# Kernel optimization log

Measured on AMD Instinct MI355X. Metric: run time of the kernel, lower is better.

The kernel has to match this reference:

```python
import jax, jax.numpy as jnp
import numpy as np

B, T, D = 2, 4096, 512
H = 8  # heads; head_dim = D // H = 64


def setup_inputs() -> dict:
    key = jax.random.key(0)
    ks = jax.random.split(key, 8)
    s = 0.02
    return {
        "queries": jax.random.normal(ks[0], (B, T, D), jnp.float32),
        "keys": jax.random.normal(ks[1], (B, T, D), jnp.float32),
        "values": jax.random.normal(ks[2], (B, T, D), jnp.float32),
        "Wq": jax.random.normal(ks[3], (D, D), jnp.float32) * s,
        "Wk": jax.random.normal(ks[4], (D, D), jnp.float32) * s,
        "Wv": jax.random.normal(ks[5], (D, D), jnp.float32) * s,
        "Wo": jax.random.normal(ks[6], (D, D), jnp.float32) * s,
        "bo": jnp.zeros((D,), jnp.float32),
    }


def reference(queries, keys, values, Wq, Wk, Wv, Wo, bo):
    # pad_dim = 0 for in_dim=512, n_heads=8, so no padding needed.
    Bq, Tq, _ = queries.shape
    Ts = keys.shape[1]
    hd = D // H
    # torch Linear: x @ W.T
    q = (queries @ Wq.T).reshape(Bq, Tq, H, hd).transpose(0, 2, 1, 3)  # [B,H,T,hd]
    k = (keys @ Wk.T).reshape(Bq, Ts, H, hd).transpose(0, 2, 1, 3)
    v = (values @ Wv.T).reshape(Bq, Ts, H, hd).transpose(0, 2, 1, 3)
    attn = jnp.einsum("bhtd,bhsd->bhts", q, k) / np.sqrt(hd).astype(np.float32)
    attn = jax.nn.softmax(attn, axis=-1)  # [B,H,T,Ts]
    z = jnp.einsum("bhts,bhsd->bhtd", attn, v)
    z = z.transpose(0, 2, 1, 3).reshape(Bq, Tq, D)
    out = z @ Wo.T + bo
    return (out, attn)
```

## Files before the change

kernel.cpp:

```cpp
#include <hip/hip_runtime.h>

typedef __attribute__((ext_vector_type(8))) short bf16x8;
typedef __attribute__((ext_vector_type(8))) unsigned short u16x8;
typedef __attribute__((ext_vector_type(4))) float f32x4;
typedef __attribute__((ext_vector_type(2))) unsigned uint2v;
typedef __attribute__((ext_vector_type(4))) unsigned uint4v;

#define DEVINL __device__ __forceinline__

constexpr int TB = 2;
constexpr int TT = 4096;
constexpr int TD = 512;
constexpr int TH = 8;
constexpr int THD = 64;
constexpr int TM = TB * TT;

DEVINL unsigned short f2b(float f) {
  unsigned u = __builtin_bit_cast(unsigned, f);
  u += 0x7FFFu + ((u >> 16) & 1u);
  return (unsigned short)(u >> 16);
}

DEVINL unsigned cvtpk(float lo, float hi) {
  unsigned r;
  asm("v_cvt_pk_bf16_f32 %0, %1, %2" : "=v"(r) : "v"(lo), "v"(hi));
  return r;
}

DEVINL void lgkm_barrier() {
  asm volatile("s_waitcnt lgkmcnt(0)" ::: "memory");
  __builtin_amdgcn_s_barrier();
  __builtin_amdgcn_sched_barrier(0);
}

__global__ __launch_bounds__(256, 2)
void proj_qkv(const float* __restrict__ Xq, const float* __restrict__ Xk,
              const float* __restrict__ Xv, const float* __restrict__ Wq,
              const float* __restrict__ Wk, const float* __restrict__ Wv,
              unsigned short* __restrict__ qb, unsigned short* __restrict__ kb,
              unsigned short* __restrict__ vt)
{
  constexpr int K = TD, N = TD;
  __shared__ unsigned short As[128][72];
  __shared__ unsigned short Bs[128][72];

  const int z = blockIdx.z;
  const float* X = (z == 0) ? Xq : (z == 1) ? Xk : Xv;
  const float* W = (z == 0) ? Wq : (z == 1) ? Wk : Wv;
  unsigned short* Yb = (z == 0) ? qb : (z == 1) ? kb : vt;
  const bool TR = (z == 2);

  const int t    = threadIdx.x;
  const int lane = t & 63, w = t >> 6;
  const int fr = lane & 15, fq = lane >> 4;
  const int wr = (w >> 1) * 64, wc = (w & 1) * 64;
  const int bm = blockIdx.x * 128, bn = blockIdx.y * 128;
  const int srow = t >> 1;
  const int skh  = (t & 1) * 32;

  f32x4 acc[4][4];
  #pragma unroll
  for (int i = 0; i < 4; ++i)
    #pragma unroll
    for (int j = 0; j < 4; ++j)
      acc[i][j] = f32x4{0.f, 0.f, 0.f, 0.f};

  for (int k0 = 0; k0 < K; k0 += 64) {
    const float* srcA = X + (size_t)(bm + srow) * K + k0 + skh;
    const float* srcB = W + (size_t)(bn + srow) * K + k0 + skh;
    #pragma unroll
    for (int i = 0; i < 4; ++i) {
      float4 a0 = ((const float4*)srcA)[2 * i];
      float4 a1 = ((const float4*)srcA)[2 * i + 1];
      u16x8 oa = {f2b(a0.x), f2b(a0.y), f2b(a0.z), f2b(a0.w),
                  f2b(a1.x), f2b(a1.y), f2b(a1.z), f2b(a1.w)};
      *(u16x8*)&As[srow][skh + i * 8] = oa;
      float4 b0 = ((const float4*)srcB)[2 * i];
      float4 b1 = ((const float4*)srcB)[2 * i + 1];
      u16x8 ob = {f2b(b0.x), f2b(b0.y), f2b(b0.z), f2b(b0.w),
                  f2b(b1.x), f2b(b1.y), f2b(b1.z), f2b(b1.w)};
      *(u16x8*)&Bs[srow][skh + i * 8] = ob;
    }
    __syncthreads();
    #pragma unroll
    for (int kk = 0; kk < 2; ++kk) {
      bf16x8 af[4], bfv[4];
      #pragma unroll
      for (int i = 0; i < 4; ++i)
        af[i] = *(const bf16x8*)&As[wr + i * 16 + fr][kk * 32 + fq * 8];
      #pragma unroll
      for (int j = 0; j < 4; ++j)
        bfv[j] = *(const bf16x8*)&Bs[wc + j * 16 + fr][kk * 32 + fq * 8];
      if (TR) {
        #pragma unroll
        for (int i = 0; i < 4; ++i)
          #pragma unroll
          for (int j = 0; j < 4; ++j)
            acc[i][j] = __builtin_amdgcn_mfma_f32_16x16x32_bf16(bfv[i], af[j], acc[i][j], 0, 0, 0);
      } else {
        #pragma unroll
        for (int i = 0; i < 4; ++i)
          #pragma unroll
          for (int j = 0; j < 4; ++j)
            acc[i][j] = __builtin_amdgcn_mfma_f32_16x16x32_bf16(af[i], bfv[j], acc[i][j], 0, 0, 0);
      }
    }
    __syncthreads();
  }

  if (TR) {
    #pragma unroll
    for (int i = 0; i < 4; ++i)
      #pragma unroll
      for (int j = 0; j < 4; ++j)
        #pragma unroll
        for (int ii = 0; ii < 4; ++ii) {
          const int Nidx = bn + wc + i * 16 + fq * 4 + ii;
          const int Midx = bm + wr + j * 16 + fr;
          const int h = Nidx >> 6, dd = Nidx & (THD - 1);
          const int b = Midx >> 12, tt = Midx & (TT - 1);
          Yb[((size_t)(b * TH + h) * THD + dd) * TT + tt] = f2b(acc[i][j][ii]);
        }
  } else {
    #pragma unroll
    for (int i = 0; i < 4; ++i)
      #pragma unroll
      for (int j = 0; j < 4; ++j)
        #pragma unroll
        for (int ii = 0; ii < 4; ++ii) {
          const int gm = bm + wr + i * 16 + fq * 4 + ii;
          const int gn = bn + wc + j * 16 + fr;
          Yb[(size_t)gm * N + gn] = f2b(acc[i][j][ii]);
        }
  }
}

__global__ __launch_bounds__(256, 2)
void gemm_final(const float* __restrict__ X, const float* __restrict__ W,
                float* __restrict__ Yf, const float* __restrict__ bias)
{
  constexpr int K = TD, N = TD;
  __shared__ unsigned short As[128][72];
  __shared__ unsigned short Bs[128][72];

  const int t    = threadIdx.x;
  const int lane = t & 63, w = t >> 6;
  const int fr = lane & 15, fq = lane >> 4;
  const int wr = (w >> 1) * 64, wc = (w & 1) * 64;
  const int bm = blockIdx.x * 128, bn = blockIdx.y * 128;
  const int srow = t >> 1;
  const int skh  = (t & 1) * 32;

  f32x4 acc[4][4];
  #pragma unroll
  for (int i = 0; i < 4; ++i)
    #pragma unroll
    for (int j = 0; j < 4; ++j)
      acc[i][j] = f32x4{0.f, 0.f, 0.f, 0.f};

  for (int k0 = 0; k0 < K; k0 += 64) {
    const float* srcA = X + (size_t)(bm + srow) * K + k0 + skh;
    const float* srcB = W + (size_t)(bn + srow) * K + k0 + skh;
    #pragma unroll
    for (int i = 0; i < 4; ++i) {
      float4 a0 = ((const float4*)srcA)[2 * i];
      float4 a1 = ((const float4*)srcA)[2 * i + 1];
      u16x8 oa = {f2b(a0.x), f2b(a0.y), f2b(a0.z), f2b(a0.w),
                  f2b(a1.x), f2b(a1.y), f2b(a1.z), f2b(a1.w)};
      *(u16x8*)&As[srow][skh + i * 8] = oa;
      float4 b0 = ((const float4*)srcB)[2 * i];
      float4 b1 = ((const float4*)srcB)[2 * i + 1];
      u16x8 ob = {f2b(b0.x), f2b(b0.y), f2b(b0.z), f2b(b0.w),
                  f2b(b1.x), f2b(b1.y), f2b(b1.z), f2b(b1.w)};
      *(u16x8*)&Bs[srow][skh + i * 8] = ob;
    }
    __syncthreads();
    #pragma unroll
    for (int kk = 0; kk < 2; ++kk) {
      bf16x8 af[4], bfv[4];
      #pragma unroll
      for (int i = 0; i < 4; ++i)
        af[i] = *(const bf16x8*)&As[wr + i * 16 + fr][kk * 32 + fq * 8];
      #pragma unroll
      for (int j = 0; j < 4; ++j)
        bfv[j] = *(const bf16x8*)&Bs[wc + j * 16 + fr][kk * 32 + fq * 8];
      #pragma unroll
      for (int i = 0; i < 4; ++i)
        #pragma unroll
        for (int j = 0; j < 4; ++j)
          acc[i][j] = __builtin_amdgcn_mfma_f32_16x16x32_bf16(af[i], bfv[j], acc[i][j], 0, 0, 0);
    }
    __syncthreads();
  }

  #pragma unroll
  for (int i = 0; i < 4; ++i)
    #pragma unroll
    for (int j = 0; j < 4; ++j)
      #pragma unroll
      for (int ii = 0; ii < 4; ++ii) {
        const int gm = bm + wr + i * 16 + fq * 4 + ii;
        const int gn = bn + wc + j * 16 + fr;
        Yf[(size_t)gm * N + gn] = acc[i][j][ii] + bias[gn];
      }
}

__global__ __launch_bounds__(256, 4)
void attn_pass1(const unsigned short* __restrict__ Qb,
                const unsigned short* __restrict__ Kb,
                const unsigned short* __restrict__ VTg,
                float* __restrict__ Z, float* __restrict__ l2iW)
{
  __shared__ unsigned short Ks[2][32][72];
  __shared__ unsigned short VTs[2][64][40];

  const int t    = threadIdx.x;
  const int lane = t & 63, w = t >> 6;
  const int fr = lane & 15, fq = lane >> 4;

  const int d  = blockIdx.x;
  const int bh = 2 * (d & 7) + ((d >> 3) & 1);
  const int q0 = (d >> 4) * 64;
  const int b  = bh >> 3, h = bh & 7;

  const size_t rowKV  = ((size_t)(b * TT)) * TD + h * THD;
  const size_t vtBase = (size_t)bh * THD * TT;

  const int trK = t >> 3, tcK = (t & 7) * 8;
  const int trV = t >> 2, tcV = (t & 3) * 8;

  auto loadK = [&](int kv0, u16x8& r) {
    r = *(const u16x8*)(Kb + rowKV + (size_t)(kv0 + trK) * TD + tcK);
  };
  auto loadVT = [&](int kv0, u16x8& r) {
    r = *(const u16x8*)(VTg + vtBase + (size_t)trV * TT + kv0 + tcV);
  };
  auto writeK  = [&](int buf, const u16x8& r) { *(u16x8*)&Ks[buf][trK][tcK]  = r; };
  auto writeVT = [&](int buf, const u16x8& r) { *(u16x8*)&VTs[buf][trV][tcV] = r; };

  const unsigned short* qsrc = Qb + ((size_t)(b * TT + q0 + w * 16 + fr)) * TD + h * THD;
  bf16x8 aq[2];
  aq[0] = *(const bf16x8*)(qsrc + fq * 8);
  aq[1] = *(const bf16x8*)(qsrc + 32 + fq * 8);

  constexpr int KVB = 32;
  constexpr int NT = TT / KVB;
  constexpr float K2 = 0.18033688011112042f;

  u16x8 kA, vA, kB, vB;
  {
    u16x8 k0, v0;
    loadK(0, k0); loadVT(0, v0);
    writeK(0, k0); writeVT(0, v0);
    loadK(KVB, kB); loadVT(KVB, vB);
    lgkm_barrier();
  }

  float lsum = 0.f;
  f32x4 accz[4];
  #pragma unroll
  for (int n = 0; n < 4; ++n) accz[n] = f32x4{0.f, 0.f, 0.f, 0.f};

  for (int jp = 0; jp < NT / 2; ++jp) {
    #pragma unroll
    for (int half = 0; half < 2; ++half) {
      const int j = jp * 2 + half;
      const int cur = j & 1;
      if (j + 2 < NT) {
        if (half == 0) { loadK((j + 2) * KVB, kA); loadVT((j + 2) * KVB, vA); }
        else           { loadK((j + 2) * KVB, kB); loadVT((j + 2) * KVB, vB); }
      }
      f32x4 sv[2];
      __builtin_amdgcn_s_setprio(1);
      #pragma unroll
      for (int n = 0; n < 2; ++n) {
        f32x4 s = f32x4{0.f, 0.f, 0.f, 0.f};
        #pragma unroll
        for (int kk = 0; kk < 2; ++kk) {
          bf16x8 ak = *(const bf16x8*)&Ks[cur][n * 16 + fr][kk * 32 + fq * 8];
          s = __builtin_amdgcn_mfma_f32_16x16x32_bf16(ak, aq[kk], s, 0, 0, 0);
        }
        sv[n] = s;
      }
      __builtin_amdgcn_s_setprio(0);
      float p[2][4];
      #pragma unroll
      for (int n = 0; n < 2; ++n)
        #pragma unroll
        for (int i = 0; i < 4; ++i) {
          p[n][i] = __builtin_amdgcn_exp2f(sv[n][i] * K2);
          lsum += p[n][i];
        }
      uint4v pav = {cvtpk(p[0][0], p[0][1]), cvtpk(p[0][2], p[0][3]),
                    cvtpk(p[1][0], p[1][1]), cvtpk(p[1][2], p[1][3])};
      bf16x8 ap = __builtin_bit_cast(bf16x8, pav);
      __builtin_amdgcn_s_setprio(1);
      #pragma unroll
      for (int df = 0; df < 4; ++df) {
        uint2v lo = *(const uint2v*)&VTs[cur][df * 16 + fr][fq * 4];
        uint2v hi = *(const uint2v*)&VTs[cur][df * 16 + fr][16 + fq * 4];
        uint4v bvv = {lo[0], lo[1], hi[0], hi[1]};
        accz[df] = __builtin_amdgcn_mfma_f32_16x16x32_bf16(
            ap, __builtin_bit_cast(bf16x8, bvv), accz[df], 0, 0, 0);
      }
      __builtin_amdgcn_s_setprio(0);
      if (j + 1 < NT) {
        if (half == 0) { writeK(cur ^ 1, kB); writeVT(cur ^ 1, vB); }
        else           { writeK(cur ^ 1, kA); writeVT(cur ^ 1, vA); }
      }
      lgkm_barrier();
    }
  }

  lsum += __shfl_xor(lsum, 16, 64);
  lsum += __shfl_xor(lsum, 32, 64);

  if (fq == 0)
    l2iW[(size_t)bh * TT + q0 + w * 16 + fr] = -__log2f(lsum);

  float rls[4];
  #pragma unroll
  for (int i = 0; i < 4; ++i)
    rls[i] = 1.0f / __shfl(lsum, fq * 4 + i, 64);
  const size_t zbase = ((size_t)(b * TT + q0 + w * 16 + fq * 4)) * TD + h * THD + fr;
  #pragma unroll
  for (int df = 0; df < 4; ++df)
    #pragma unroll
    for (int i = 0; i < 4; ++i)
      Z[zbase + (size_t)i * TD + df * 16] = accz[df][i] * rls[i];
}

__global__ __launch_bounds__(256, 4)
void attn_pass2(const unsigned short* __restrict__ Qb,
                const unsigned short* __restrict__ Kb,
                const float* __restrict__ l2iW,
                float* __restrict__ attnO)
{
  __shared__ unsigned short KsW[4][2][32][72];

  const int t    = threadIdx.x;
  const int lane = t & 63, w = t >> 6;
  const int fr = lane & 15, fq = lane >> 4;

  const int d  = blockIdx.x;
  const int bh = 2 * (d & 7) + ((d >> 3) & 1);
  const int q0 = (d >> 4) * 64;
  const int b  = bh >> 3, h = bh & 7;

  const size_t rowKV = ((size_t)(b * TT)) * TD + h * THD;

  const unsigned short* qsrc = Qb + ((size_t)(b * TT + q0 + w * 16 + fr)) * TD + h * THD;
  bf16x8 aq[2];
  aq[0] = *(const bf16x8*)(qsrc + fq * 8);
  aq[1] = *(const bf16x8*)(qsrc + 32 + fq * 8);

  const float l2i = l2iW[(size_t)bh * TT + q0 + w * 16 + fr];

  constexpr int KVB = 32;
  constexpr int NT = TT / KVB;
  constexpr float K2 = 0.18033688011112042f;

  const int phase = (37 * d + 32 * w) & (NT - 1);
  const int prow = lane >> 3, pcol = (lane & 7) * 8;

  u16x8 sA[4], sB[4];
  auto loadKW = [&](int kvt, u16x8* s) {
    #pragma unroll
    for (int i = 0; i < 4; ++i)
      s[i] = *(const u16x8*)(Kb + rowKV +
               (size_t)(kvt * KVB + i * 8 + prow) * TD + pcol);
  };
  auto writeKW = [&](int buf, const u16x8* s) {
    #pragma unroll
    for (int i = 0; i < 4; ++i)
      *(u16x8*)&KsW[w][buf][i * 8 + prow][pcol] = s[i];
  };
  auto PH = [&](int jj) { return (jj + phase) & (NT - 1); };

  float* arow = attnO + ((size_t)bh * TT + q0 + w * 16 + fr) * TT + fq * 4;

#define P2_COMPUTE(JJ, BUF)                                                    \
  {                                                                            \
    const int j = PH(JJ);                                                      \
    f32x4 sv[2];                                                               \
    __builtin_amdgcn_s_setprio(1);                                             \
    _Pragma("unroll")                                                          \
    for (int n = 0; n < 2; ++n) {                                              \
      f32x4 s = f32x4{0.f, 0.f, 0.f, 0.f};                                     \
      _Pragma("unroll")                                                        \
      for (int kk = 0; kk < 2; ++kk) {                                         \
        bf16x8 ak = *(const bf16x8*)&KsW[w][(BUF)][n * 16 + fr][kk * 32 + fq * 8]; \
        s = __builtin_amdgcn_mfma_f32_16x16x32_bf16(ak, aq[kk], s, 0, 0, 0);   \
      }                                                                        \
      sv[n] = s;                                                               \
    }                                                                          \
    __builtin_amdgcn_s_setprio(0);                                             \
    _Pragma("unroll")                                                          \
    for (int n = 0; n < 2; ++n) {                                              \
      f32x4 pv4 = {__builtin_amdgcn_exp2f(fmaf(sv[n][0], K2, l2i)),            \
                   __builtin_amdgcn_exp2f(fmaf(sv[n][1], K2, l2i)),            \
                   __builtin_amdgcn_exp2f(fmaf(sv[n][2], K2, l2i)),            \
                   __builtin_amdgcn_exp2f(fmaf(sv[n][3], K2, l2i))};           \
      *(f32x4*)(arow + j * KVB + n * 16) = pv4;                                \
    }                                                                          \
  }

  loadKW(PH(0), sA);
  writeKW(0, sA);
  loadKW(PH(1), sB);

  for (int jp = 0; jp < NT / 2; ++jp) {
    const int jj0 = 2 * jp;
    if (jj0 + 2 < NT) loadKW(PH(jj0 + 2), sA);
    P2_COMPUTE(jj0, 0)
    writeKW(1, sB);
    if (jj0 + 3 < NT) loadKW(PH(jj0 + 3), sB);
    P2_COMPUTE(jj0 + 1, 1)
    if (jj0 + 2 < NT) writeKW(0, sA);
  }
#undef P2_COMPUTE
}

extern "C" void kernel_launch(void* const* d_in, const int* in_sizes, int n_in,
                              void* d_out, int out_size, void* d_ws, size_t ws_size,
                              hipStream_t stream) {
  const float* queries = (const float*)d_in[0];
  const float* keys    = (const float*)d_in[1];
  const float* values  = (const float*)d_in[2];
  const float* Wq = (const float*)d_in[3];
  const float* Wk = (const float*)d_in[4];
  const float* Wv = (const float*)d_in[5];
  const float* Wo = (const float*)d_in[6];
  const float* bo = (const float*)d_in[7];

  float* out  = (float*)d_out;
  float* attn = out + (size_t)TM * TD;

  unsigned short* qb = (unsigned short*)d_ws;
  unsigned short* kb = qb + (size_t)TM * TD;
  unsigned short* vt = kb + (size_t)TM * TD;
  float*          zf = (float*)(vt + (size_t)TM * TD);
  float*          l2iW = zf + (size_t)TM * TD;

  proj_qkv<<<dim3(TM / 128, TD / 128, 3), 256, 0, stream>>>(
      queries, keys, values, Wq, Wk, Wv, qb, kb, vt);

  attn_pass1<<<dim3(1024), 256, 0, stream>>>(qb, kb, vt, zf, l2iW);

  attn_pass2<<<dim3(1024), 256, 0, stream>>>(qb, kb, l2iW, attn);

  gemm_final<<<dim3(TM / 128, TD / 128), 256, 0, stream>>>(zf, Wo, out, bo);
}
```

Measured before the change: 490.7 us.

## Merge output projection GEMM into attention pass2 launch and load K directly to registers

Combines the final Wo projection GEMM and the attention-probability pass into one launch: the first 512 blocks run a 128x64-tile GEMM while the remaining 1024 blocks write the softmax probabilities, so the small GEMM can overlap the store-bound pass2. Pass2 also drops its per-wave LDS staging of K and loads MFMA fragments straight from global memory into registers with double buffering. This removes one launch and the LDS round trip. The cost is a larger shared-memory footprint for all blocks and uncoalesced fragment loads that rely on cache reuse.

```diff
diff --git a/kernel.cpp b/kernel.cpp
--- a/kernel.cpp
+++ b/kernel.cpp
@@ -135,76 +135,6 @@
   }
 }
 
-__global__ __launch_bounds__(256, 2)
-void gemm_final(const float* __restrict__ X, const float* __restrict__ W,
-                float* __restrict__ Yf, const float* __restrict__ bias)
-{
-  constexpr int K = TD, N = TD;
-  __shared__ unsigned short As[128][72];
-  __shared__ unsigned short Bs[128][72];
-
-  const int t    = threadIdx.x;
-  const int lane = t & 63, w = t >> 6;
-  const int fr = lane & 15, fq = lane >> 4;
-  const int wr = (w >> 1) * 64, wc = (w & 1) * 64;
-  const int bm = blockIdx.x * 128, bn = blockIdx.y * 128;
-  const int srow = t >> 1;
-  const int skh  = (t & 1) * 32;
-
-  f32x4 acc[4][4];
-  #pragma unroll
-  for (int i = 0; i < 4; ++i)
-    #pragma unroll
-    for (int j = 0; j < 4; ++j)
-      acc[i][j] = f32x4{0.f, 0.f, 0.f, 0.f};
-
-  for (int k0 = 0; k0 < K; k0 += 64) {
-    const float* srcA = X + (size_t)(bm + srow) * K + k0 + skh;
-    const float* srcB = W + (size_t)(bn + srow) * K + k0 + skh;
-    #pragma unroll
-    for (int i = 0; i < 4; ++i) {
-      float4 a0 = ((const float4*)srcA)[2 * i];
-      float4 a1 = ((const float4*)srcA)[2 * i + 1];
-      u16x8 oa = {f2b(a0.x), f2b(a0.y), f2b(a0.z), f2b(a0.w),
-                  f2b(a1.x), f2b(a1.y), f2b(a1.z), f2b(a1.w)};
-      *(u16x8*)&As[srow][skh + i * 8] = oa;
-      float4 b0 = ((const float4*)srcB)[2 * i];
-      float4 b1 = ((const float4*)srcB)[2 * i + 1];
-      u16x8 ob = {f2b(b0.x), f2b(b0.y), f2b(b0.z), f2b(b0.w),
-                  f2b(b1.x), f2b(b1.y), f2b(b1.z), f2b(b1.w)};
-      *(u16x8*)&Bs[srow][skh + i * 8] = ob;
-    }
-    __syncthreads();
-    #pragma unroll
-    for (int kk = 0; kk < 2; ++kk) {
-      bf16x8 af[4], bfv[4];
-      #pragma unroll
-      for (int i = 0; i < 4; ++i)
-        af[i] = *(const bf16x8*)&As[wr + i * 16 + fr][kk * 32 + fq * 8];
-      #pragma unroll
-      for (int j = 0; j < 4; ++j)
-        bfv[j] = *(const bf16x8*)&Bs[wc + j * 16 + fr][kk * 32 + fq * 8];
-      #pragma unroll
-      for (int i = 0; i < 4; ++i)
-        #pragma unroll
-        for (int j = 0; j < 4; ++j)
-          acc[i][j] = __builtin_amdgcn_mfma_f32_16x16x32_bf16(af[i], bfv[j], acc[i][j], 0, 0, 0);
-    }
-    __syncthreads();
-  }
-
-  #pragma unroll
-  for (int i = 0; i < 4; ++i)
-    #pragma unroll
-    for (int j = 0; j < 4; ++j)
-      #pragma unroll
-      for (int ii = 0; ii < 4; ++ii) {
-        const int gm = bm + wr + i * 16 + fq * 4 + ii;
-        const int gn = bn + wc + j * 16 + fr;
-        Yf[(size_t)gm * N + gn] = acc[i][j][ii] + bias[gn];
-      }
-}
-
 __global__ __launch_bounds__(256, 4)
 void attn_pass1(const unsigned short* __restrict__ Qb,
                 const unsigned short* __restrict__ Kb,
@@ -331,28 +261,95 @@
 }
 
 __global__ __launch_bounds__(256, 4)
-void attn_pass2(const unsigned short* __restrict__ Qb,
+void pass2_gemm(const unsigned short* __restrict__ Qb,
                 const unsigned short* __restrict__ Kb,
                 const float* __restrict__ l2iW,
-                float* __restrict__ attnO)
+                float* __restrict__ attnO,
+                const float* __restrict__ Zf,
+                const float* __restrict__ Wo,
+                const float* __restrict__ bo,
+                float* __restrict__ outO)
 {
-  __shared__ unsigned short KsW[4][2][32][72];
+  __shared__ __align__(16) char smem_[27648];
 
   const int t    = threadIdx.x;
   const int lane = t & 63, w = t >> 6;
   const int fr = lane & 15, fq = lane >> 4;
-
   const int d  = blockIdx.x;
-  const int bh = 2 * (d & 7) + ((d >> 3) & 1);
-  const int q0 = (d >> 4) * 64;
+
+  if (d < 512) {
+    auto GAs = (unsigned short (*)[72])smem_;
+    auto GBs = (unsigned short (*)[72])(smem_ + 18432);
+    const int gm0 = (d >> 3) * 128, gn0 = (d & 7) * 64;
+    const int wr = (w >> 1) * 64, wc = (w & 1) * 32;
+    const int srow = t >> 1, skh = (t & 1) * 32;
+    const int brow = t >> 2, bkh = (t & 3) * 16;
+    f32x4 gacc[4][2];
+    #pragma unroll
+    for (int i = 0; i < 4; ++i)
+      #pragma unroll
+      for (int j = 0; j < 2; ++j)
+        gacc[i][j] = f32x4{0.f, 0.f, 0.f, 0.f};
+    for (int k0 = 0; k0 < TD; k0 += 64) {
+      const float* srcA = Zf + (size_t)(gm0 + srow) * TD + k0 + skh;
+      #pragma unroll
+      for (int i = 0; i < 4; ++i) {
+        float4 a0 = ((const float4*)srcA)[2 * i];
+        float4 a1 = ((const float4*)srcA)[2 * i + 1];
+        u16x8 oa = {f2b(a0.x), f2b(a0.y), f2b(a0.z), f2b(a0.w),
+                    f2b(a1.x), f2b(a1.y), f2b(a1.z), f2b(a1.w)};
+        *(u16x8*)&GAs[srow][skh + i * 8] = oa;
+      }
+      const float* srcB = Wo + (size_t)(gn0 + brow) * TD + k0 + bkh;
+      #pragma unroll
+      for (int i = 0; i < 2; ++i) {
+        float4 b0 = ((const float4*)srcB)[2 * i];
+        float4 b1 = ((const float4*)srcB)[2 * i + 1];
+        u16x8 ob = {f2b(b0.x), f2b(b0.y), f2b(b0.z), f2b(b0.w),
+                    f2b(b1.x), f2b(b1.y), f2b(b1.z), f2b(b1.w)};
+        *(u16x8*)&GBs[brow][bkh + i * 8] = ob;
+      }
+      __syncthreads();
+      #pragma unroll
+      for (int kk = 0; kk < 2; ++kk) {
+        bf16x8 af[4], bfv[2];
+        #pragma unroll
+        for (int i = 0; i < 4; ++i)
+          af[i] = *(const bf16x8*)&GAs[wr + i * 16 + fr][kk * 32 + fq * 8];
+        #pragma unroll
+        for (int j = 0; j < 2; ++j)
+          bfv[j] = *(const bf16x8*)&GBs[wc + j * 16 + fr][kk * 32 + fq * 8];
+        #pragma unroll
+        for (int i = 0; i < 4; ++i)
+          #pragma unroll
+          for (int j = 0; j < 2; ++j)
+            gacc[i][j] = __builtin_amdgcn_mfma_f32_16x16x32_bf16(af[i], bfv[j], gacc[i][j], 0, 0, 0);
+      }
+      __syncthreads();
+    }
+    #pragma unroll
+    for (int i = 0; i < 4; ++i)
+      #pragma unroll
+      for (int j = 0; j < 2; ++j)
+        #pragma unroll
+        for (int ii = 0; ii < 4; ++ii) {
+          const int gm = gm0 + wr + i * 16 + fq * 4 + ii;
+          const int gn = gn0 + wc + j * 16 + fr;
+          outO[(size_t)gm * TD + gn] = gacc[i][j][ii] + bo[gn];
+        }
+    return;
+  }
+
+  const int ds = d - 512;
+  const int bh = 2 * (ds & 7) + ((ds >> 3) & 1);
+  const int q0 = (ds >> 4) * 64;
   const int b  = bh >> 3, h = bh & 7;
 
   const size_t rowKV = ((size_t)(b * TT)) * TD + h * THD;
 
   const unsigned short* qsrc = Qb + ((size_t)(b * TT + q0 + w * 16 + fr)) * TD + h * THD;
-  bf16x8 aq[2];
-  aq[0] = *(const bf16x8*)(qsrc + fq * 8);
-  aq[1] = *(const bf16x8*)(qsrc + 32 + fq * 8);
+  bf16x8 aq0 = *(const bf16x8*)(qsrc + fq * 8);
+  bf16x8 aq1 = *(const bf16x8*)(qsrc + 32 + fq * 8);
 
   const float l2i = l2iW[(size_t)bh * TT + q0 + w * 16 + fr];
 
@@ -360,65 +357,51 @@
   constexpr int NT = TT / KVB;
   constexpr float K2 = 0.18033688011112042f;
 
-  const int phase = (37 * d + 32 * w) & (NT - 1);
-  const int prow = lane >> 3, pcol = (lane & 7) * 8;
-
-  u16x8 sA[4], sB[4];
-  auto loadKW = [&](int kvt, u16x8* s) {
-    #pragma unroll
-    for (int i = 0; i < 4; ++i)
-      s[i] = *(const u16x8*)(Kb + rowKV +
-               (size_t)(kvt * KVB + i * 8 + prow) * TD + pcol);
+  const int phase = (37 * ds + 32 * w) & (NT - 1);
+  auto PH = [&](int jj) { return (jj + phase) & (NT - 1); };
+
+  const unsigned short* kfb = Kb + rowKV + (size_t)fr * TD + fq * 8;
+  auto LD = [&](int j, u16x8* f) {
+    const unsigned short* p = kfb + (size_t)(j * KVB) * TD;
+    f[0] = *(const u16x8*)(p);
+    f[1] = *(const u16x8*)(p + 32);
+    f[2] = *(const u16x8*)(p + (size_t)16 * TD);
+    f[3] = *(const u16x8*)(p + (size_t)16 * TD + 32);
   };
-  auto writeKW = [&](int buf, const u16x8* s) {
-    #pragma unroll
-    for (int i = 0; i < 4; ++i)
-      *(u16x8*)&KsW[w][buf][i * 8 + prow][pcol] = s[i];
-  };
-  auto PH = [&](int jj) { return (jj + phase) & (NT - 1); };
 
   float* arow = attnO + ((size_t)bh * TT + q0 + w * 16 + fr) * TT + fq * 4;
 
-#define P2_COMPUTE(JJ, BUF)                                                    \
+#define P2C(JJ, F)                                                             \
   {                                                                            \
     const int j = PH(JJ);                                                      \
-    f32x4 sv[2];                                                               \
+    f32x4 s0 = f32x4{0.f, 0.f, 0.f, 0.f}, s1 = f32x4{0.f, 0.f, 0.f, 0.f};      \
     __builtin_amdgcn_s_setprio(1);                                             \
-    _Pragma("unroll")                                                          \
-    for (int n = 0; n < 2; ++n) {                                              \
-      f32x4 s = f32x4{0.f, 0.f, 0.f, 0.f};                                     \
-      _Pragma("unroll")                                                        \
-      for (int kk = 0; kk < 2; ++kk) {                                         \
-        bf16x8 ak = *(const bf16x8*)&KsW[w][(BUF)][n * 16 + fr][kk * 32 + fq * 8]; \
-        s = __builtin_amdgcn_mfma_f32_16x16x32_bf16(ak, aq[kk], s, 0, 0, 0);   \
-      }                                                                        \
-      sv[n] = s;                                                               \
-    }                                                                          \
+    s0 = __builtin_amdgcn_mfma_f32_16x16x32_bf16(__builtin_bit_cast(bf16x8, F[0]), aq0, s0, 0, 0, 0); \
+    s0 = __builtin_amdgcn_mfma_f32_16x16x32_bf16(__builtin_bit_cast(bf16x8, F[1]), aq1, s0, 0, 0, 0); \
+    s1 = __builtin_amdgcn_mfma_f32_16x16x32_bf16(__builtin_bit_cast(bf16x8, F[2]), aq0, s1, 0, 0, 0); \
+    s1 = __builtin_amdgcn_mfma_f32_16x16x32_bf16(__builtin_bit_cast(bf16x8, F[3]), aq1, s1, 0, 0, 0); \
     __builtin_amdgcn_s_setprio(0);                                             \
-    _Pragma("unroll")                                                          \
-    for (int n = 0; n < 2; ++n) {                                              \
-      f32x4 pv4 = {__builtin_amdgcn_exp2f(fmaf(sv[n][0], K2, l2i)),            \
-                   __builtin_amdgcn_exp2f(fmaf(sv[n][1], K2, l2i)),            \
-                   __builtin_amdgcn_exp2f(fmaf(sv[n][2], K2, l2i)),            \
-                   __builtin_amdgcn_exp2f(fmaf(sv[n][3], K2, l2i))};           \
-      *(f32x4*)(arow + j * KVB + n * 16) = pv4;                                \
-    }                                                                          \
-  }
-
-  loadKW(PH(0), sA);
-  writeKW(0, sA);
-  loadKW(PH(1), sB);
-
-  for (int jp = 0; jp < NT / 2; ++jp) {
-    const int jj0 = 2 * jp;
-    if (jj0 + 2 < NT) loadKW(PH(jj0 + 2), sA);
-    P2_COMPUTE(jj0, 0)
-    writeKW(1, sB);
-    if (jj0 + 3 < NT) loadKW(PH(jj0 + 3), sB);
-    P2_COMPUTE(jj0 + 1, 1)
-    if (jj0 + 2 < NT) writeKW(0, sA);
-  }
-#undef P2_COMPUTE
+    f32x4 pv0 = {__builtin_amdgcn_exp2f(fmaf(s0[0], K2, l2i)),                 \
+                 __builtin_amdgcn_exp2f(fmaf(s0[1], K2, l2i)),                 \
+                 __builtin_amdgcn_exp2f(fmaf(s0[2], K2, l2i)),                 \
+                 __builtin_amdgcn_exp2f(fmaf(s0[3], K2, l2i))};                \
+    *(f32x4*)(arow + j * KVB) = pv0;                                           \
+    f32x4 pv1 = {__builtin_amdgcn_exp2f(fmaf(s1[0], K2, l2i)),                 \
+                 __builtin_amdgcn_exp2f(fmaf(s1[1], K2, l2i)),                 \
+                 __builtin_amdgcn_exp2f(fmaf(s1[2], K2, l2i)),                 \
+                 __builtin_amdgcn_exp2f(fmaf(s1[3], K2, l2i))};                \
+    *(f32x4*)(arow + j * KVB + 16) = pv1;                                      \
+  }
+
+  u16x8 fA[4], fB[4];
+  LD(PH(0), fA);
+  for (int jj = 0; jj < NT; jj += 2) {
+    if (jj + 1 < NT) LD(PH(jj + 1), fB);
+    P2C(jj, fA)
+    if (jj + 2 < NT) LD(PH(jj + 2), fA);
+    P2C(jj + 1, fB)
+  }
+#undef P2C
 }
 
 extern "C" void kernel_launch(void* const* d_in, const int* in_sizes, int n_in,
@@ -447,7 +430,6 @@
 
   attn_pass1<<<dim3(1024), 256, 0, stream>>>(qb, kb, vt, zf, l2iW);
 
-  attn_pass2<<<dim3(1024), 256, 0, stream>>>(qb, kb, l2iW, attn);
-
-  gemm_final<<<dim3(TM / 128, TD / 128), 256, 0, stream>>>(zf, Wo, out, bo);
-}
+  pass2_gemm<<<dim3(1536), 256, 0, stream>>>(qb, kb, l2iW, attn,
+                                             zf, Wo, bo, out);
+}
```

Result: slower. 549.5 us (+12.0%).

## Split attention pass1 over two KV halves and reduce partials in new kernel

Applied to the files above, without the earlier changes.

Pass1 now splits each query tile's KV range into two halves, giving twice as many blocks (2048). Each block writes unnormalized partial Z accumulators and row sums to scratch space borrowed from the attn output buffer. A new reduce_z kernel then adds the two halves, normalizes, and writes Z and the log-sum values. Launch bounds rise to 6 blocks per CU to improve occupancy. The split costs an extra kernel launch and extra global traffic for the partials. Combining halves without a running max stays valid only because the softmax appears to use a fixed scale with no max subtraction.

```diff
diff --git a/kernel.cpp b/kernel.cpp
--- a/kernel.cpp
+++ b/kernel.cpp
@@ -205,11 +205,11 @@
       }
 }
 
-__global__ __launch_bounds__(256, 4)
-void attn_pass1(const unsigned short* __restrict__ Qb,
-                const unsigned short* __restrict__ Kb,
-                const unsigned short* __restrict__ VTg,
-                float* __restrict__ Z, float* __restrict__ l2iW)
+__global__ __launch_bounds__(256, 6)
+void attn_pass1p(const unsigned short* __restrict__ Qb,
+                 const unsigned short* __restrict__ Kb,
+                 const unsigned short* __restrict__ VTg,
+                 float* __restrict__ acczP, float* __restrict__ lsumP)
 {
   __shared__ unsigned short Ks[2][32][72];
   __shared__ unsigned short VTs[2][64][40];
@@ -219,9 +219,11 @@
   const int fr = lane & 15, fq = lane >> 4;
 
   const int d  = blockIdx.x;
-  const int bh = 2 * (d & 7) + ((d >> 3) & 1);
-  const int q0 = (d >> 4) * 64;
+  const int ds = d >> 1, kh = d & 1;
+  const int bh = 2 * (ds & 7) + ((ds >> 3) & 1);
+  const int q0 = (ds >> 4) * 64;
   const int b  = bh >> 3, h = bh & 7;
+  const int kvBase = kh * (TT / 2);
 
   const size_t rowKV  = ((size_t)(b * TT)) * TD + h * THD;
   const size_t vtBase = (size_t)bh * THD * TT;
@@ -230,10 +232,10 @@
   const int trV = t >> 2, tcV = (t & 3) * 8;
 
   auto loadK = [&](int kv0, u16x8& r) {
-    r = *(const u16x8*)(Kb + rowKV + (size_t)(kv0 + trK) * TD + tcK);
+    r = *(const u16x8*)(Kb + rowKV + (size_t)(kvBase + kv0 + trK) * TD + tcK);
   };
   auto loadVT = [&](int kv0, u16x8& r) {
-    r = *(const u16x8*)(VTg + vtBase + (size_t)trV * TT + kv0 + tcV);
+    r = *(const u16x8*)(VTg + vtBase + (size_t)trV * TT + kvBase + kv0 + tcV);
   };
   auto writeK  = [&](int buf, const u16x8& r) { *(u16x8*)&Ks[buf][trK][tcK]  = r; };
   auto writeVT = [&](int buf, const u16x8& r) { *(u16x8*)&VTs[buf][trV][tcV] = r; };
@@ -244,7 +246,7 @@
   aq[1] = *(const bf16x8*)(qsrc + 32 + fq * 8);
 
   constexpr int KVB = 32;
-  constexpr int NT = TT / KVB;
+  constexpr int NT = TT / 2 / KVB;
   constexpr float K2 = 0.18033688011112042f;
 
   u16x8 kA, vA, kB, vB;
@@ -314,20 +316,46 @@
 
   lsum += __shfl_xor(lsum, 16, 64);
   lsum += __shfl_xor(lsum, 32, 64);
-
   if (fq == 0)
-    l2iW[(size_t)bh * TT + q0 + w * 16 + fr] = -__log2f(lsum);
-
-  float rls[4];
-  #pragma unroll
-  for (int i = 0; i < 4; ++i)
-    rls[i] = 1.0f / __shfl(lsum, fq * 4 + i, 64);
-  const size_t zbase = ((size_t)(b * TT + q0 + w * 16 + fq * 4)) * TD + h * THD + fr;
+    lsumP[(size_t)d * 64 + w * 16 + fr] = lsum;
+
+  float* ab = acczP + (size_t)d * 4096 + (size_t)(w * 16 + fq * 4) * 64 + fr;
   #pragma unroll
   for (int df = 0; df < 4; ++df)
     #pragma unroll
     for (int i = 0; i < 4; ++i)
-      Z[zbase + (size_t)i * TD + df * 16] = accz[df][i] * rls[i];
+      ab[(size_t)i * 64 + df * 16] = accz[df][i];
+}
+
+__global__ __launch_bounds__(256, 8)
+void reduce_z(const float* __restrict__ acczP, const float* __restrict__ lsumP,
+              float* __restrict__ Z, float* __restrict__ l2iW)
+{
+  const int ds = blockIdx.x;
+  const int bh = 2 * (ds & 7) + ((ds >> 3) & 1);
+  const int q0 = (ds >> 4) * 64;
+  const int b  = bh >> 3, h = bh & 7;
+
+  const int t = threadIdx.x;
+  const int q = t >> 2, c0 = (t & 3) * 16;
+
+  const float l = lsumP[(size_t)(2 * ds) * 64 + q] +
+                  lsumP[(size_t)(2 * ds + 1) * 64 + q];
+  const float rinv = 1.0f / l;
+  if ((t & 3) == 0)
+    l2iW[(size_t)bh * TT + q0 + q] = -__log2f(l);
+
+  const float* a0 = acczP + (size_t)(2 * ds) * 4096 + (size_t)q * 64 + c0;
+  const float* a1 = acczP + (size_t)(2 * ds + 1) * 4096 + (size_t)q * 64 + c0;
+  float* zdst = Z + (size_t)(b * TT + q0 + q) * TD + h * THD + c0;
+  #pragma unroll
+  for (int i = 0; i < 4; ++i) {
+    f32x4 v0 = *(const f32x4*)(a0 + i * 4);
+    f32x4 v1 = *(const f32x4*)(a1 + i * 4);
+    f32x4 r = {(v0[0] + v1[0]) * rinv, (v0[1] + v1[1]) * rinv,
+               (v0[2] + v1[2]) * rinv, (v0[3] + v1[3]) * rinv};
+    *(f32x4*)(zdst + i * 4) = r;
+  }
 }
 
 __global__ __launch_bounds__(256, 4)
@@ -442,10 +470,15 @@
   float*          zf = (float*)(vt + (size_t)TM * TD);
   float*          l2iW = zf + (size_t)TM * TD;
 
+  float* acczP = attn;
+  float* lsumP = attn + (size_t)2048 * 4096;
+
   proj_qkv<<<dim3(TM / 128, TD / 128, 3), 256, 0, stream>>>(
       queries, keys, values, Wq, Wk, Wv, qb, kb, vt);
 
-  attn_pass1<<<dim3(1024), 256, 0, stream>>>(qb, kb, vt, zf, l2iW);
+  attn_pass1p<<<dim3(2048), 256, 0, stream>>>(qb, kb, vt, acczP, lsumP);
+
+  reduce_z<<<dim3(1024), 256, 0, stream>>>(acczP, lsumP, zf, l2iW);
 
   attn_pass2<<<dim3(1024), 256, 0, stream>>>(qb, kb, l2iW, attn);
 
```

New measurement: 518.7 us. +5.7%, slower.
